# Optimization experiments

Hardware: AMD Instinct MI355X
Metric: run time of the kernel (lower is better)

## Reference

```python
import jax, jax.numpy as jnp
import numpy as np

B, N_PER, D = 128, 512, 128        # graphs, nodes per graph, feature width
N = B * N_PER                      # 65536 total nodes
E = 524288                         # total edges (avg degree 8)
KS = (410, 328, 263)               # ceil(0.8*512), ceil(0.8*410), ceil(0.8*328)


def setup_inputs() -> dict:
    key = jax.random.key(0)
    ks = jax.random.split(key, 20)
    p = lambda k, shape: jax.random.normal(k, shape, jnp.float32) * 0.05
    rng = np.random.default_rng(0)
    g = rng.integers(0, B, size=E)
    s = rng.integers(0, N_PER, size=E)
    t = rng.integers(0, N_PER, size=E)
    edge_index = jnp.asarray(np.stack([g * N_PER + s, g * N_PER + t]).astype(np.int32))
    inp = {
        'x': jax.random.normal(ks[0], (N, 1, D), jnp.float32),
        'edge_index': edge_index,
    }
    i = 1
    for l in (1, 2, 3):
        inp[f'conv{l}_wl'] = p(ks[i], (D, D)); i += 1   # SAGEConv lin_l (neighbors) weight
        inp[f'conv{l}_bl'] = p(ks[i], (D,));  i += 1   # SAGEConv lin_l bias
        inp[f'conv{l}_wr'] = p(ks[i], (D, D)); i += 1   # SAGEConv lin_r (root) weight
        inp[f'pool{l}_w'] = p(ks[i], (D,));   i += 1   # TopKPooling score vector
    inp['lin1_w'] = p(ks[13], (128, 256)); inp['lin1_b'] = p(ks[14], (128,))
    inp['lin2_w'] = p(ks[15], (64, 128));  inp['lin2_b'] = p(ks[16], (64,))
    inp['lin3_w'] = p(ks[17], (1, 64));    inp['lin3_b'] = p(ks[18], (1,))
    return inp


def _sage(x, node_mask, src, dst, wl, bl, wr):
    # SAGEConv, mean aggregation: lin_l(mean_{j->i} x_j) + lin_r(x_i)
    em = (node_mask[src] & node_mask[dst]).astype(x.dtype)   # [E] valid-edge mask
    msum = jax.ops.segment_sum(x[src] * em[:, None], dst, num_segments=N)
    deg = jax.ops.segment_sum(em, dst, num_segments=N)
    mean = msum / jnp.maximum(deg, 1.0)[:, None]
    return mean @ wl.T + bl + x @ wr.T


def _topk_pool(x, node_mask, w, k):
    # TopKPooling: score = x.w/||w||; keep top-k per graph; gate kept x by tanh(score)
    score = (x @ w) / (jnp.linalg.norm(w) + 1e-16)           # [N]
    score = jnp.where(node_mask, score, -jnp.inf)
    _, idx = jax.lax.top_k(score.reshape(B, N_PER), k)       # [B, k] within-graph ids
    nm = jnp.zeros((B, N_PER), bool).at[jnp.arange(B)[:, None], idx].set(True).reshape(-1)
    x = jnp.where(nm[:, None], x * jnp.tanh(score)[:, None], 0.0)
    return x, nm


def _readout(x, node_mask, k):
    # cat([global_max_pool, global_mean_pool]) over the k surviving nodes per graph
    xb = x.reshape(B, N_PER, -1)
    mb = node_mask.reshape(B, N_PER, 1)
    gmax = jnp.max(jnp.where(mb, xb, -jnp.inf), axis=1)
    gmean = jnp.sum(jnp.where(mb, xb, 0.0), axis=1) / k
    return jnp.concatenate([gmax, gmean], axis=1)            # [B, 2D]


def _forward(edge_index, x, conv1_wl, conv1_bl, conv1_wr, pool1_w,
             conv2_wl, conv2_bl, conv2_wr, pool2_w,
             conv3_wl, conv3_bl, conv3_wr, pool3_w,
             lin1_w, lin1_b, lin2_w, lin2_b, lin3_w, lin3_b):
    src, dst = edge_index[0], edge_index[1]
    h = x[:, 0, :]                                           # x.squeeze(1) -> [N, D]
    nm = jnp.ones((N,), bool)
    layers = ((conv1_wl, conv1_bl, conv1_wr, pool1_w),
              (conv2_wl, conv2_bl, conv2_wr, pool2_w),
              (conv3_wl, conv3_bl, conv3_wr, pool3_w))
    reads = []
    for (wl, bl, wr, pw), k in zip(layers, KS):
        h = jax.nn.relu(_sage(h, nm, src, dst, wl, bl, wr))
        h, nm = _topk_pool(h, nm, pw, k)
        reads.append(_readout(h, nm, float(k)))
    z = reads[0] + reads[1] + reads[2]                       # [B, 256]
    z = jax.nn.relu(z @ lin1_w.T + lin1_b)
    z = jax.nn.relu(z @ lin2_w.T + lin2_b)
    # dropout p=0.5 is a no-op at eval time
    return jax.nn.sigmoid(z @ lin3_w.T + lin3_b)[:, 0]       # [B]


def reference(x, edge_index, conv1_wl, conv1_bl, conv1_wr, pool1_w,
              conv2_wl, conv2_bl, conv2_wr, pool2_w,
              conv3_wl, conv3_bl, conv3_wr, pool3_w,
              lin1_w, lin1_b, lin2_w, lin2_b, lin3_w, lin3_b):
    return _forward(edge_index, x, conv1_wl, conv1_bl, conv1_wr, pool1_w,
                    conv2_wl, conv2_bl, conv2_wr, pool2_w,
                    conv3_wl, conv3_bl, conv3_wr, pool3_w,
                    lin1_w, lin1_b, lin2_w, lin2_b, lin3_w, lin3_b)
```

## Files before the change

kernel.cpp:

```cpp
#include <hip/hip_runtime.h>
#include <math.h>

#define NND 65536
#define NPER 512
#define NGR 128
#define DD 128
#define NED 524288

typedef __attribute__((ext_vector_type(8))) short short8;
typedef __attribute__((ext_vector_type(4))) float f32x4;

__device__ __forceinline__ unsigned short f2b(float f) {
  unsigned u = __float_as_uint(f);
  return (unsigned short)((u + 0x7FFFu + ((u >> 16) & 1u)) >> 16);
}
__device__ __forceinline__ float b2f(unsigned short h) {
  return __uint_as_float(((unsigned)h) << 16);
}


__global__ __launch_bounds__(256) void init_prepw_kernel(
    int* __restrict__ counts, float2* __restrict__ tm,
    const float* __restrict__ wl0, const float* __restrict__ wr0,
    const float* __restrict__ wl1, const float* __restrict__ wr1,
    const float* __restrict__ wl2, const float* __restrict__ wr2,
    unsigned short* __restrict__ Whi, unsigned short* __restrict__ Wlo) {
  const int bid = blockIdx.x;
  if (bid < 256) {
    int i = bid * 256 + threadIdx.x;
    counts[i] = 0;
    tm[i] = make_float2(1.f, 1.f);
    return;
  }
  const float* wls[3] = {wl0, wl1, wl2};
  const float* wrs[3] = {wr0, wr1, wr2};
  int e = (bid - 256) * 256 + threadIdx.x;
  int l = e >> 15;
  int o = e & 32767;
  int j = o & 7;
  int lane = (o >> 3) & 63;
  int nt = (o >> 9) & 7;
  int kc = o >> 12;
  int li = lane & 15, q = lane >> 4;
  int n = nt * 16 + li;
  int k = kc * 32 + q * 8 + j;
  const float* src = (k < 128) ? wls[l] : wrs[l];
  float v = src[n * DD + (k & 127)];
  unsigned short hi = f2b(v);
  float lo = v - b2f(hi);
  Whi[e] = hi;
  Wlo[e] = f2b(lo);
}

__global__ __launch_bounds__(256) void hist_kernel(const int* __restrict__ ei,
                                                   int* __restrict__ counts) {
  int e = blockIdx.x * 256 + threadIdx.x;
  atomicAdd(&counts[ei[NED + e]], 1);
}


__global__ __launch_bounds__(256) void scan1_kernel(const int* __restrict__ counts,
                                                    int* __restrict__ csum) {
  __shared__ int ws[4];
  const int b = blockIdx.x;
  const int t = threadIdx.x;
  const int4 v = ((const int4*)(counts + b * 1024))[t];
  int s = v.x + v.y + v.z + v.w;
#pragma unroll
  for (int o = 32; o > 0; o >>= 1) s += __shfl_down(s, o);
  if ((t & 63) == 0) ws[t >> 6] = s;
  __syncthreads();
  if (t == 0) csum[b] = ws[0] + ws[1] + ws[2] + ws[3];
}

__global__ __launch_bounds__(256) void scan2_kernel(const int* __restrict__ counts,
                                                    const int* __restrict__ csum,
                                                    int* __restrict__ off,
                                                    int* __restrict__ cursor) {
  __shared__ int s_part[256];
  __shared__ int s_base;
  const int b = blockIdx.x;
  const int t = threadIdx.x;
  const int4 v = ((const int4*)(counts + b * 1024))[t];
  const int s = v.x + v.y + v.z + v.w;
  s_part[t] = s;
  if (t < 64) {
    int val = (t < b) ? csum[t] : 0;
#pragma unroll
    for (int o = 32; o > 0; o >>= 1) val += __shfl_down(val, o);
    if (t == 0) s_base = val;
  }
  __syncthreads();
  for (int d = 1; d < 256; d <<= 1) {
    int val = (t >= d) ? s_part[t - d] : 0;
    __syncthreads();
    s_part[t] += val;
    __syncthreads();
  }
  const int excl = s_base + ((t == 0) ? 0 : s_part[t - 1]);
  int4 o4;
  o4.x = excl;
  o4.y = excl + v.x;
  o4.z = o4.y + v.y;
  o4.w = o4.z + v.z;
  ((int4*)(off + b * 1024))[t] = o4;
  ((int4*)(cursor + b * 1024))[t] = o4;
  if (b == 0 && t == 0) off[NND] = NED;
}

__global__ __launch_bounds__(256) void scatter_kernel(const int* __restrict__ ei,
                                                      int* __restrict__ cursor,
                                                      int* __restrict__ ssrc) {
  int e = blockIdx.x * 256 + threadIdx.x;
  int dst = ei[NED + e];
  int pos = atomicAdd(&cursor[dst], 1);
  ssrc[pos] = ei[e];
}


__global__ __launch_bounds__(256) void pe_kernel(const int* __restrict__ ssrc,
                                                 const float2* __restrict__ tm,
                                                 float* __restrict__ pet,
                                                 unsigned long long* __restrict__ plive) {
  const int e = blockIdx.x * 256 + threadIdx.x;
  const int s = ssrc[e];
  const float2 mt = tm[s];
  const int lv = (mt.x != 0.f) ? 1 : 0;
  pet[e] = lv ? mt.y : 0.f;
  const unsigned long long bl = __ballot(lv);
  if ((threadIdx.x & 63) == 0) plive[e >> 6] = bl;
}


template <int CM>
__global__ __launch_bounds__(256) void agg_kernel_t(
    const float* __restrict__ x, const float2* __restrict__ tm,
    const int* __restrict__ off, const int* __restrict__ ssrc,
    const float* __restrict__ pet, const unsigned long long* __restrict__ plive,
    unsigned short* __restrict__ mhi, unsigned short* __restrict__ mlo) {
  const int wave = threadIdx.x >> 6;
  const int lane = threadIdx.x & 63;
  const int half = lane >> 5;
  const int l = lane & 31;
  const int bid = blockIdx.x;
  const int xcd = bid & 7;
  const int slot = bid >> 3;
  const int graph = xcd * 16 + (slot >> 5);
  const int within = slot & 31;
  const int d0 = graph * NPER + within * 16 + wave * 4;

  int offv = 0;
  if (lane < 5) offv = off[d0 + lane];
  float deadv = 1.f;
  if (CM && lane < 4) deadv = tm[d0 + lane].x;
  const int b0 = __shfl(offv, 0);
  const int b1 = __shfl(offv, 1);
  const int b2 = __shfl(offv, 2);
  const int b3 = __shfl(offv, 3);
  const int e3 = __shfl(offv, 4);
  float dd[4];
  if (CM) {
    dd[0] = __shfl(deadv, 0);
    dd[1] = __shfl(deadv, 1);
    dd[2] = __shfl(deadv, 2);
    dd[3] = __shfl(deadv, 3);
  }
  const int begs[4] = {b0, b1, b2, b3};
  const int ends[4] = {b1, b2, b3, e3};

  float4 acc[4];
  int deg[4];
#pragma unroll
  for (int d = 0; d < 4; ++d) {
    acc[d] = make_float4(0.f, 0.f, 0.f, 0.f);
    deg[d] = 0;
  }

  for (int wbase = b0 & ~63; wbase < e3; wbase += 64) {
    const int sv = ssrc[wbase + lane];
    float tv = 0.f;
    unsigned long long lm = 0;
    if (CM) {
      tv = pet[wbase + lane];
      lm = plive[wbase >> 6];
    }

#pragma unroll
    for (int d = 0; d < 4; ++d) {
      if (CM && dd[d] == 0.f) continue;
      const int lo = max(begs[d], wbase);
      const int hi = min(ends[d], wbase + 64);
      if (lo >= hi) continue;
      const int j0 = lo - wbase;
      const int j1 = hi - wbase;
      if (CM) {
        const unsigned long long wm =
            (((j1 == 64) ? ~0ull : ((1ull << j1) - 1)) & ~((1ull << j0) - 1));
        deg[d] += (int)__popcll(lm & wm);
      } else {
        deg[d] += j1 - j0;
      }
      int j = j0 + half;
      for (; j + 6 < j1; j += 8) {
        const int s0 = __shfl(sv, j);
        const int s1 = __shfl(sv, j + 2);
        const int s2 = __shfl(sv, j + 4);
        const int s3 = __shfl(sv, j + 6);
        const float4 v0 = *(const float4*)(x + (size_t)s0 * DD + l * 4);
        const float4 v1 = *(const float4*)(x + (size_t)s1 * DD + l * 4);
        const float4 v2 = *(const float4*)(x + (size_t)s2 * DD + l * 4);
        const float4 v3 = *(const float4*)(x + (size_t)s3 * DD + l * 4);
        if (CM) {
          const float t0 = __shfl(tv, j), t1 = __shfl(tv, j + 2);
          const float t2 = __shfl(tv, j + 4), t3 = __shfl(tv, j + 6);
          acc[d].x += v0.x * t0 + v1.x * t1 + v2.x * t2 + v3.x * t3;
          acc[d].y += v0.y * t0 + v1.y * t1 + v2.y * t2 + v3.y * t3;
          acc[d].z += v0.z * t0 + v1.z * t1 + v2.z * t2 + v3.z * t3;
          acc[d].w += v0.w * t0 + v1.w * t1 + v2.w * t2 + v3.w * t3;
        } else {
          acc[d].x += v0.x + v1.x + v2.x + v3.x;
          acc[d].y += v0.y + v1.y + v2.y + v3.y;
          acc[d].z += v0.z + v1.z + v2.z + v3.z;
          acc[d].w += v0.w + v1.w + v2.w + v3.w;
        }
      }
      for (; j < j1; j += 2) {
        const int s = __shfl(sv, j);
        const float4 v = *(const float4*)(x + (size_t)s * DD + l * 4);
        if (CM) {
          const float t = __shfl(tv, j);
          acc[d].x += v.x * t;
          acc[d].y += v.y * t;
          acc[d].z += v.z * t;
          acc[d].w += v.w * t;
        } else {
          acc[d].x += v.x;
          acc[d].y += v.y;
          acc[d].z += v.z;
          acc[d].w += v.w;
        }
      }
    }
  }

#pragma unroll
  for (int d = 0; d < 4; ++d) {
    if (CM && dd[d] == 0.f) continue;
    float4 a = acc[d];
    a.x += __shfl(a.x, lane ^ 32);
    a.y += __shfl(a.y, lane ^ 32);
    a.z += __shfl(a.z, lane ^ 32);
    a.w += __shfl(a.w, lane ^ 32);
    if (lane < 32) {
      const float inv = 1.f / (float)max(deg[d], 1);
      float4 m;
      m.x = a.x * inv;
      m.y = a.y * inv;
      m.z = a.z * inv;
      m.w = a.w * inv;
      ushort4 hv, lv;
      hv.x = f2b(m.x); lv.x = f2b(m.x - b2f(hv.x));
      hv.y = f2b(m.y); lv.y = f2b(m.y - b2f(hv.y));
      hv.z = f2b(m.z); lv.z = f2b(m.z - b2f(hv.z));
      hv.w = f2b(m.w); lv.w = f2b(m.w - b2f(hv.w));
      const size_t ad = (size_t)(d0 + d) * DD + l * 4;
      *(ushort4*)(mhi + ad) = hv;
      *(ushort4*)(mlo + ad) = lv;
    }
  }
}


#define GBM 64

template <int SCALE>
__global__ __launch_bounds__(256) void gemm_kernel_t(
    const unsigned short* __restrict__ Amh, const unsigned short* __restrict__ Aml,
    const float* __restrict__ Ax, const float2* __restrict__ tmp,
    const unsigned short* __restrict__ Whi, const unsigned short* __restrict__ Wlo,
    const float* __restrict__ bias, const float* __restrict__ pw,
    float* __restrict__ outp, float* __restrict__ sraw) {
  __shared__ short Ah[4096];
  __shared__ short Al[4096];
  __shared__ float s_sp[4][GBM];
  const int tid = threadIdx.x;
  const int wv = tid >> 6;
  const int lane = tid & 63;
  const int q = lane >> 4;
  const int li = lane & 15;
  const int row0 = blockIdx.x * GBM;

  int sdst[2];
#pragma unroll
  for (int i = 0; i < 2; ++i) {
    const int id = tid + i * 256;
    const int r = id >> 3;
    const int kb = (id & 7) << 2;
    sdst[i] = ((r >> 4) * 64 + (kb >> 3) * 16 + (r & 15)) * 8 + (kb & 7);
  }

  f32x4 acc[4][2];
#pragma unroll
  for (int m = 0; m < 4; ++m)
#pragma unroll
    for (int n = 0; n < 2; ++n) acc[m][n] = (f32x4){0.f, 0.f, 0.f, 0.f};

  float4 pa[2];
  ushort4 pmh[2], pml[2];
  short8 pbh[2], pbl[2];

#define LOADA(KC)                                                                      \
  {                                                                                    \
    if ((KC) < 4) {                                                                    \
      const int cb = (KC)*32;                                                          \
      _Pragma("unroll") for (int i = 0; i < 2; ++i) {                                  \
        const int id = tid + i * 256;                                                  \
        const size_t ga = (size_t)(row0 + (id >> 3)) * DD + cb + ((id & 7) << 2);      \
        pmh[i] = *(const ushort4*)(Amh + ga);                                          \
        pml[i] = *(const ushort4*)(Aml + ga);                                          \
      }                                                                                \
    } else {                                                                           \
      const int cb = ((KC)&3) * 32;                                                    \
      _Pragma("unroll") for (int i = 0; i < 2; ++i) {                                  \
        const int id = tid + i * 256;                                                  \
        pa[i] = *(const float4*)(Ax + (size_t)(row0 + (id >> 3)) * DD + cb + ((id & 7) << 2)); \
        if (SCALE) {                                                                   \
          const float tt = tmp[row0 + (id >> 3)].y;                                    \
          pa[i].x *= tt; pa[i].y *= tt; pa[i].z *= tt; pa[i].w *= tt;                  \
        }                                                                              \
      }                                                                                \
    }                                                                                  \
  }
#define LOADB(KC)                                                                      \
  {                                                                                    \
    _Pragma("unroll") for (int n = 0; n < 2; ++n) {                                    \
      const int ga = (((KC)*8 + wv * 2 + n) * 64 + lane) * 8;                          \
      pbh[n] = *(const short8*)(Whi + ga);                                             \
      pbl[n] = *(const short8*)(Wlo + ga);                                             \
    }                                                                                  \
  }
#define STAGE(KC)                                                                      \
  {                                                                                    \
    short* Adh = Ah + ((KC)&1) * 2048;                                                 \
    short* Adl = Al + ((KC)&1) * 2048;                                                 \
    if ((KC) < 4) {                                                                    \
      _Pragma("unroll") for (int i = 0; i < 2; ++i) {                                  \
        *(ushort4*)(Adh + sdst[i]) = pmh[i];                                           \
        *(ushort4*)(Adl + sdst[i]) = pml[i];                                           \
      }                                                                                \
    } else {                                                                           \
      _Pragma("unroll") for (int i = 0; i < 2; ++i) {                                  \
        ushort4 hv, lv;                                                                \
        hv.x = f2b(pa[i].x); lv.x = f2b(pa[i].x - b2f(hv.x));                          \
        hv.y = f2b(pa[i].y); lv.y = f2b(pa[i].y - b2f(hv.y));                          \
        hv.z = f2b(pa[i].z); lv.z = f2b(pa[i].z - b2f(hv.z));                          \
        hv.w = f2b(pa[i].w); lv.w = f2b(pa[i].w - b2f(hv.w));                          \
        *(ushort4*)(Adh + sdst[i]) = hv;                                               \
        *(ushort4*)(Adl + sdst[i]) = lv;                                               \
      }                                                                                \
    }                                                                                  \
  }

  LOADA(0) LOADB(0)
  STAGE(0)
  LOADA(1)

#pragma unroll
  for (int kc = 0; kc < 8; ++kc) {
    short8 bh[2], bl[2];
    bh[0] = pbh[0]; bh[1] = pbh[1];
    bl[0] = pbl[0]; bl[1] = pbl[1];
    __syncthreads();
    short8 ah[4], al[4];
    const short* Ash = Ah + (kc & 1) * 2048;
    const short* Asl = Al + (kc & 1) * 2048;
#pragma unroll
    for (int m = 0; m < 4; ++m) {
      ah[m] = *(const short8*)(Ash + (m * 64 + lane) * 8);
      al[m] = *(const short8*)(Asl + (m * 64 + lane) * 8);
    }
    switch (kc) {
      case 0: STAGE(1) LOADB(1) LOADA(2) break;
      case 1: STAGE(2) LOADB(2) LOADA(3) break;
      case 2: STAGE(3) LOADB(3) LOADA(4) break;
      case 3: STAGE(4) LOADB(4) LOADA(5) break;
      case 4: STAGE(5) LOADB(5) LOADA(6) break;
      case 5: STAGE(6) LOADB(6) LOADA(7) break;
      case 6: STAGE(7) LOADB(7) break;
      default: break;
    }
#pragma unroll
    for (int m = 0; m < 4; ++m)
#pragma unroll
      for (int n = 0; n < 2; ++n) {
        acc[m][n] = __builtin_amdgcn_mfma_f32_16x16x32_bf16(ah[m], bh[n], acc[m][n], 0, 0, 0);
        acc[m][n] = __builtin_amdgcn_mfma_f32_16x16x32_bf16(ah[m], bl[n], acc[m][n], 0, 0, 0);
        acc[m][n] = __builtin_amdgcn_mfma_f32_16x16x32_bf16(al[m], bh[n], acc[m][n], 0, 0, 0);
      }
  }
#undef LOADA
#undef LOADB
#undef STAGE

  const int c0 = wv * 32 + li;
  const int c1 = wv * 32 + 16 + li;
  const float b0 = bias[c0], b1 = bias[c1];
  const float p0 = pw[c0], p1 = pw[c1];
  float sp[16];
#pragma unroll
  for (int m = 0; m < 4; ++m) {
#pragma unroll
    for (int i = 0; i < 4; ++i) {
      const int r = row0 + m * 16 + q * 4 + i;
      const float v0 = fmaxf(acc[m][0][i] + b0, 0.f);
      const float v1 = fmaxf(acc[m][1][i] + b1, 0.f);
      outp[(size_t)r * DD + c0] = v0;
      outp[(size_t)r * DD + c1] = v1;
      sp[m * 4 + i] = v0 * p0 + v1 * p1;
    }
  }
#pragma unroll
  for (int e = 0; e < 16; ++e) {
    sp[e] += __shfl_xor(sp[e], 1);
    sp[e] += __shfl_xor(sp[e], 2);
    sp[e] += __shfl_xor(sp[e], 4);
    sp[e] += __shfl_xor(sp[e], 8);
  }
  if (li == 0) {
#pragma unroll
    for (int e = 0; e < 16; ++e) s_sp[wv][(e >> 2) * 16 + q * 4 + (e & 3)] = sp[e];
  }
  __syncthreads();
  if (tid < GBM)
    sraw[row0 + tid] = s_sp[0][tid] + s_sp[1][tid] + s_sp[2][tid] + s_sp[3][tid];
}


__global__ __launch_bounds__(256) void pool_kernel(const float* __restrict__ h,
                                                   const float* __restrict__ sraw,
                                                   const float* __restrict__ pw,
                                                   const float2* __restrict__ tmP,
                                                   float2* __restrict__ tmN,
                                                   float* __restrict__ zp,
                                                   const int kk) {
  __shared__ float s_sc[NPER];
  __shared__ float s_t[128];
  __shared__ unsigned char s_sel[128];
  __shared__ int s_rk[256];
  __shared__ float4 red4[512];
  __shared__ float s_norm;
  const int b = blockIdx.x;
  const int g = b >> 2;
  const int q = b & 3;
  const int tid = threadIdx.x;
  const int lane = tid & 63;

  if (tid < 64) {
    const float v0 = pw[lane], v1 = pw[lane + 64];
    float p = v0 * v0 + v1 * v1;
#pragma unroll
    for (int o = 32; o > 0; o >>= 1) p += __shfl_down(p, o);
    if (lane == 0) s_norm = 1.f / (sqrtf(p) + 1e-16f);
  }
  __syncthreads();
  const float inv_norm = s_norm;
#pragma unroll
  for (int i = 0; i < 2; ++i) {
    const int n = tid + i * 256;
    const int node = g * NPER + n;
    s_sc[n] = (tmP[node].x != 0.f) ? sraw[node] * inv_norm : -INFINITY;
  }
  __syncthreads();

  {
    const int n = q * 128 + (tid & 127);
    const int jb = (tid >> 7) * 256;
    const float s = s_sc[n];
    int rank = 0;
    for (int j = jb; j < jb + 256; ++j) {
      const float sj = s_sc[j];
      rank += (sj > s || (sj == s && j < n)) ? 1 : 0;
    }
    s_rk[tid] = rank;
  }
  __syncthreads();
  if (tid < 128) {
    const int n = q * 128 + tid;
    const int rank = s_rk[tid] + s_rk[tid + 128];
    const int sel = (rank < kk) ? 1 : 0;
    const float s = s_sc[n];
    const float t = sel ? tanhf(s) : 0.f;
    tmN[g * NPER + n] = make_float2(sel ? 1.f : 0.f, t);
    s_sel[tid] = (unsigned char)sel;
    s_t[tid] = t;
  }
  __syncthreads();

  const int c = tid & 31;
  const int r = tid >> 5;
  float4 pmax = make_float4(-INFINITY, -INFINITY, -INFINITY, -INFINITY);
  float4 psum = make_float4(0.f, 0.f, 0.f, 0.f);
  const size_t nbase = (size_t)g * NPER + q * 128;
  const float4* h4 = (const float4*)h;
  for (int i = 0; i < 16; ++i) {
    const int nl = r + 8 * i;
    if (s_sel[nl]) {
      float4 v = h4[(nbase + nl) * 32 + c];
      const float t = s_t[nl];
      v.x *= t; v.y *= t; v.z *= t; v.w *= t;
      pmax.x = fmaxf(pmax.x, v.x);
      pmax.y = fmaxf(pmax.y, v.y);
      pmax.z = fmaxf(pmax.z, v.z);
      pmax.w = fmaxf(pmax.w, v.w);
      psum.x += v.x; psum.y += v.y; psum.z += v.z; psum.w += v.w;
    }
  }
  red4[r * 32 + c] = pmax;
  red4[256 + r * 32 + c] = psum;
  __syncthreads();
  if (tid < 32) {
    float4 m = red4[tid];
    float4 sm = red4[256 + tid];
#pragma unroll
    for (int rr = 1; rr < 8; ++rr) {
      const float4 a = red4[rr * 32 + tid];
      const float4 s2 = red4[256 + rr * 32 + tid];
      m.x = fmaxf(m.x, a.x); m.y = fmaxf(m.y, a.y);
      m.z = fmaxf(m.z, a.z); m.w = fmaxf(m.w, a.w);
      sm.x += s2.x; sm.y += s2.y; sm.z += s2.z; sm.w += s2.w;
    }
    *(float4*)(zp + (size_t)b * 256 + tid * 4) = m;
    *(float4*)(zp + (size_t)b * 256 + 128 + tid * 4) = sm;
  }
}


__global__ __launch_bounds__(128) void mlp_kernel(const float* __restrict__ zpart,
                                                  const float* __restrict__ w1,
                                                  const float* __restrict__ b1,
                                                  const float* __restrict__ w2,
                                                  const float* __restrict__ b2,
                                                  const float* __restrict__ w3,
                                                  const float* __restrict__ b3,
                                                  float* __restrict__ out,
                                                  const float ik0, const float ik1,
                                                  const float ik2) {
  __shared__ float z[256];
  __shared__ float h1[128];
  __shared__ float h2[64];
  const int g = blockIdx.x;
  const int t = threadIdx.x;
  const float iks[3] = {ik0, ik1, ik2};
  float zmax = 0.f, zmean = 0.f;
#pragma unroll
  for (int l = 0; l < 3; ++l) {
    const float* zp = zpart + ((size_t)l * 512 + g * 4) * 256;
    zmax += fmaxf(fmaxf(zp[t], zp[256 + t]), fmaxf(zp[512 + t], zp[768 + t]));
    zmean += (zp[128 + t] + zp[384 + t] + zp[640 + t] + zp[896 + t]) * iks[l];
  }
  z[t] = zmax;
  z[128 + t] = zmean;
  __syncthreads();
  float a = b1[t];
  for (int k = 0; k < 256; ++k) a = fmaf(z[k], w1[t * 256 + k], a);
  h1[t] = fmaxf(a, 0.f);
  __syncthreads();
  if (t < 64) {
    float a2 = b2[t];
    for (int k = 0; k < 128; ++k) a2 = fmaf(h1[k], w2[t * 128 + k], a2);
    h2[t] = fmaxf(a2, 0.f);
  }
  __syncthreads();
  if (t == 0) {
    float a3 = b3[0];
    for (int k = 0; k < 64; ++k) a3 = fmaf(h2[k], w3[k], a3);
    out[g] = 1.f / (1.f + expf(-a3));
  }
}


extern "C" void kernel_launch(void* const* d_in, const int* in_sizes, int n_in,
                              void* d_out, int out_size, void* d_ws, size_t ws_size,
                              hipStream_t stream) {
  (void)in_sizes; (void)n_in; (void)out_size; (void)ws_size;
  const float* x_in = (const float*)d_in[0];
  const int* ei = (const int*)d_in[1];
  const float* wl[3] = {(const float*)d_in[2], (const float*)d_in[6], (const float*)d_in[10]};
  const float* cbl[3] = {(const float*)d_in[3], (const float*)d_in[7], (const float*)d_in[11]};
  const float* wr[3] = {(const float*)d_in[4], (const float*)d_in[8], (const float*)d_in[12]};
  const float* pw[3] = {(const float*)d_in[5], (const float*)d_in[9], (const float*)d_in[13]};
  const float* l1w = (const float*)d_in[14];
  const float* l1b = (const float*)d_in[15];
  const float* l2w = (const float*)d_in[16];
  const float* l2b = (const float*)d_in[17];
  const float* l3w = (const float*)d_in[18];
  const float* l3b = (const float*)d_in[19];
  float* out = (float*)d_out;

  char* w = (char*)d_ws;
  int* counts = (int*)(w + 0 * (1 << 20));
  int* off = (int*)(w + 1 * (1 << 20));
  int* csum = (int*)(w + 1 * (1 << 20) + (1 << 19));
  int* cursor = (int*)(w + 2 * (1 << 20));
  float* sraw = (float*)(w + 2 * (1 << 20));
  float2* tmA = (float2*)(w + 3 * (1 << 20));
  float2* tmB = (float2*)(w + 3 * (1 << 20) + (1 << 19));
  float* zpart = (float*)(w + 4 * (1 << 20));
  unsigned short* Whi = (unsigned short*)(w + 5 * (1 << 20) + (1 << 19));
  unsigned short* Wlo = (unsigned short*)(w + 5 * (1 << 20) + 3 * (1 << 18));
  int* ssrc = (int*)(w + 6 * (1 << 20));
  unsigned short* mhi = (unsigned short*)(w + (size_t)8 * (1 << 20));
  unsigned short* mlo = (unsigned short*)(w + (size_t)24 * (1 << 20));
  float* hA = (float*)(w + (size_t)40 * (1 << 20));
  float* hB = (float*)(w + (size_t)72 * (1 << 20));
  float* pet = (float*)(w + (size_t)104 * (1 << 20));
  unsigned long long* plive = (unsigned long long*)(w + (size_t)107 * (1 << 20));

  init_prepw_kernel<<<640, 256, 0, stream>>>(counts, tmA, wl[0], wr[0], wl[1], wr[1],
                                             wl[2], wr[2], Whi, Wlo);
  hist_kernel<<<NED / 256, 256, 0, stream>>>(ei, counts);
  scan1_kernel<<<64, 256, 0, stream>>>(counts, csum);
  scan2_kernel<<<64, 256, 0, stream>>>(counts, csum, off, cursor);
  scatter_kernel<<<NED / 256, 256, 0, stream>>>(ei, cursor, ssrc);

  const int ks[3] = {410, 328, 263};
  const float* xl = x_in;
  float* houts[3] = {hA, hB, hA};
  float2* tprev[3] = {tmA, tmB, tmA};
  float2* tnext[3] = {tmB, tmA, tmB};
  for (int l = 0; l < 3; ++l) {
    float* hout = houts[l];
    if (l == 0) {
      agg_kernel_t<0><<<4096, 256, 0, stream>>>(xl, tprev[l], off, ssrc, pet, plive,
                                                mhi, mlo);
      gemm_kernel_t<0><<<NND / GBM, 256, 0, stream>>>(mhi, mlo, xl, tprev[l],
                                                      Whi + (size_t)l * 32768,
                                                      Wlo + (size_t)l * 32768, cbl[l], pw[l],
                                                      hout, sraw);
    } else {
      pe_kernel<<<NED / 256, 256, 0, stream>>>(ssrc, tprev[l], pet, plive);
      agg_kernel_t<1><<<4096, 256, 0, stream>>>(xl, tprev[l], off, ssrc, pet, plive,
                                                mhi, mlo);
      gemm_kernel_t<1><<<NND / GBM, 256, 0, stream>>>(mhi, mlo, xl, tprev[l],
                                                      Whi + (size_t)l * 32768,
                                                      Wlo + (size_t)l * 32768, cbl[l], pw[l],
                                                      hout, sraw);
    }
    pool_kernel<<<NGR * 4, 256, 0, stream>>>(hout, sraw, pw[l], tprev[l], tnext[l],
                                             zpart + (size_t)l * 512 * 256, ks[l]);
    xl = hout;
  }
  mlp_kernel<<<NGR, 128, 0, stream>>>(zpart, l1w, l1b, l2w, l2b, l3w, l3b, out,
                                      1.f / 410.f, 1.f / 328.f, 1.f / 263.f);
}
```

Measured before the change: 366.7 us.

## Fuse neighbor mean aggregation into SAGE GEMM kernel via shared memory

Merges the aggregation kernel and the GEMM kernel into one kernel. Each block gathers neighbor means for 64 rows and writes the bf16 hi/lo split straight into LDS in MFMA fragment layout, so the global round trip through the mhi/mlo buffers and one launch per layer go away. Each wave now handles 16 destination nodes with 16 float4 accumulators, which raises register pressure, and the grid shrinks from 4096 to 1024 blocks with more LDS per block, which may lower occupancy and gather latency hiding. The per-node dead-node skip is also dropped, so dead destinations are still aggregated.

```diff
diff --git a/kernel.cpp b/kernel.cpp
--- a/kernel.cpp
+++ b/kernel.cpp
@@ -133,50 +133,52 @@
 
 
 template <int CM>
-__global__ __launch_bounds__(256) void agg_kernel_t(
-    const float* __restrict__ x, const float2* __restrict__ tm,
+__global__ __launch_bounds__(256) void fused_kernel_t(
+    const float* __restrict__ x, const float2* __restrict__ tmp,
     const int* __restrict__ off, const int* __restrict__ ssrc,
     const float* __restrict__ pet, const unsigned long long* __restrict__ plive,
-    unsigned short* __restrict__ mhi, unsigned short* __restrict__ mlo) {
-  const int wave = threadIdx.x >> 6;
-  const int lane = threadIdx.x & 63;
+    const unsigned short* __restrict__ Whi, const unsigned short* __restrict__ Wlo,
+    const float* __restrict__ bias, const float* __restrict__ pw,
+    float* __restrict__ outp, float* __restrict__ sraw) {
+  __shared__ short Mh[8192];
+  __shared__ short Ml[8192];
+  __shared__ short Ah[4096];
+  __shared__ short Al[4096];
+  __shared__ float s_sp[4][64];
+  const int tid = threadIdx.x;
+  const int wv = tid >> 6;
+  const int lane = tid & 63;
   const int half = lane >> 5;
   const int l = lane & 31;
+  const int q = lane >> 4;
+  const int li = lane & 15;
   const int bid = blockIdx.x;
   const int xcd = bid & 7;
-  const int slot = bid >> 3;
-  const int graph = xcd * 16 + (slot >> 5);
-  const int within = slot & 31;
-  const int d0 = graph * NPER + within * 16 + wave * 4;
-
+  const int idx = bid >> 3;
+  const int graph = xcd * 16 + (idx >> 3);
+  const int row0 = graph * NPER + (idx & 7) * 64;
+
+  const int d0 = row0 + wv * 16;
   int offv = 0;
-  if (lane < 5) offv = off[d0 + lane];
-  float deadv = 1.f;
-  if (CM && lane < 4) deadv = tm[d0 + lane].x;
-  const int b0 = __shfl(offv, 0);
-  const int b1 = __shfl(offv, 1);
-  const int b2 = __shfl(offv, 2);
-  const int b3 = __shfl(offv, 3);
-  const int e3 = __shfl(offv, 4);
-  float dd[4];
-  if (CM) {
-    dd[0] = __shfl(deadv, 0);
-    dd[1] = __shfl(deadv, 1);
-    dd[2] = __shfl(deadv, 2);
-    dd[3] = __shfl(deadv, 3);
-  }
-  const int begs[4] = {b0, b1, b2, b3};
-  const int ends[4] = {b1, b2, b3, e3};
-
-  float4 acc[4];
-  int deg[4];
-#pragma unroll
-  for (int d = 0; d < 4; ++d) {
-    acc[d] = make_float4(0.f, 0.f, 0.f, 0.f);
+  if (lane < 17) offv = off[d0 + lane];
+  int begs[16], ends[16];
+#pragma unroll
+  for (int d = 0; d < 16; ++d) {
+    begs[d] = __builtin_amdgcn_readfirstlane(__shfl(offv, d));
+    ends[d] = __builtin_amdgcn_readfirstlane(__shfl(offv, d + 1));
+  }
+  const int b0 = begs[0];
+  const int eN = ends[15];
+
+  float4 macc[16];
+  int deg[16];
+#pragma unroll
+  for (int d = 0; d < 16; ++d) {
+    macc[d] = make_float4(0.f, 0.f, 0.f, 0.f);
     deg[d] = 0;
   }
 
-  for (int wbase = b0 & ~63; wbase < e3; wbase += 64) {
+  for (int wbase = b0 & ~63; wbase < eN; wbase += 64) {
     const int sv = ssrc[wbase + lane];
     float tv = 0.f;
     unsigned long long lm = 0;
@@ -184,10 +186,8 @@
       tv = pet[wbase + lane];
       lm = plive[wbase >> 6];
     }
-
-#pragma unroll
-    for (int d = 0; d < 4; ++d) {
-      if (CM && dd[d] == 0.f) continue;
+#pragma unroll
+    for (int d = 0; d < 16; ++d) {
       const int lo = max(begs[d], wbase);
       const int hi = min(ends[d], wbase + 64);
       if (lo >= hi) continue;
@@ -213,15 +213,15 @@
         if (CM) {
           const float t0 = __shfl(tv, j), t1 = __shfl(tv, j + 2);
           const float t2 = __shfl(tv, j + 4), t3 = __shfl(tv, j + 6);
-          acc[d].x += v0.x * t0 + v1.x * t1 + v2.x * t2 + v3.x * t3;
-          acc[d].y += v0.y * t0 + v1.y * t1 + v2.y * t2 + v3.y * t3;
-          acc[d].z += v0.z * t0 + v1.z * t1 + v2.z * t2 + v3.z * t3;
-          acc[d].w += v0.w * t0 + v1.w * t1 + v2.w * t2 + v3.w * t3;
+          macc[d].x += v0.x * t0 + v1.x * t1 + v2.x * t2 + v3.x * t3;
+          macc[d].y += v0.y * t0 + v1.y * t1 + v2.y * t2 + v3.y * t3;
+          macc[d].z += v0.z * t0 + v1.z * t1 + v2.z * t2 + v3.z * t3;
+          macc[d].w += v0.w * t0 + v1.w * t1 + v2.w * t2 + v3.w * t3;
         } else {
-          acc[d].x += v0.x + v1.x + v2.x + v3.x;
-          acc[d].y += v0.y + v1.y + v2.y + v3.y;
-          acc[d].z += v0.z + v1.z + v2.z + v3.z;
-          acc[d].w += v0.w + v1.w + v2.w + v3.w;
+          macc[d].x += v0.x + v1.x + v2.x + v3.x;
+          macc[d].y += v0.y + v1.y + v2.y + v3.y;
+          macc[d].z += v0.z + v1.z + v2.z + v3.z;
+          macc[d].w += v0.w + v1.w + v2.w + v3.w;
         }
       }
       for (; j < j1; j += 2) {
@@ -229,24 +229,23 @@
         const float4 v = *(const float4*)(x + (size_t)s * DD + l * 4);
         if (CM) {
           const float t = __shfl(tv, j);
-          acc[d].x += v.x * t;
-          acc[d].y += v.y * t;
-          acc[d].z += v.z * t;
-          acc[d].w += v.w * t;
+          macc[d].x += v.x * t;
+          macc[d].y += v.y * t;
+          macc[d].z += v.z * t;
+          macc[d].w += v.w * t;
         } else {
-          acc[d].x += v.x;
-          acc[d].y += v.y;
-          acc[d].z += v.z;
-          acc[d].w += v.w;
+          macc[d].x += v.x;
+          macc[d].y += v.y;
+          macc[d].z += v.z;
+          macc[d].w += v.w;
         }
       }
     }
   }
 
 #pragma unroll
-  for (int d = 0; d < 4; ++d) {
-    if (CM && dd[d] == 0.f) continue;
-    float4 a = acc[d];
+  for (int d = 0; d < 16; ++d) {
+    float4 a = macc[d];
     a.x += __shfl(a.x, lane ^ 32);
     a.y += __shfl(a.y, lane ^ 32);
     a.z += __shfl(a.z, lane ^ 32);
@@ -263,32 +262,11 @@
       hv.y = f2b(m.y); lv.y = f2b(m.y - b2f(hv.y));
       hv.z = f2b(m.z); lv.z = f2b(m.z - b2f(hv.z));
       hv.w = f2b(m.w); lv.w = f2b(m.w - b2f(hv.w));
-      const size_t ad = (size_t)(d0 + d) * DD + l * 4;
-      *(ushort4*)(mhi + ad) = hv;
-      *(ushort4*)(mlo + ad) = lv;
-    }
-  }
-}
-
-
-#define GBM 64
-
-template <int SCALE>
-__global__ __launch_bounds__(256) void gemm_kernel_t(
-    const unsigned short* __restrict__ Amh, const unsigned short* __restrict__ Aml,
-    const float* __restrict__ Ax, const float2* __restrict__ tmp,
-    const unsigned short* __restrict__ Whi, const unsigned short* __restrict__ Wlo,
-    const float* __restrict__ bias, const float* __restrict__ pw,
-    float* __restrict__ outp, float* __restrict__ sraw) {
-  __shared__ short Ah[4096];
-  __shared__ short Al[4096];
-  __shared__ float s_sp[4][GBM];
-  const int tid = threadIdx.x;
-  const int wv = tid >> 6;
-  const int lane = tid & 63;
-  const int q = lane >> 4;
-  const int li = lane & 15;
-  const int row0 = blockIdx.x * GBM;
+      const int ad = (wv * 256 + (l >> 1) * 16 + d) * 8 + (l & 1) * 4;
+      *(ushort4*)(Mh + ad) = hv;
+      *(ushort4*)(Ml + ad) = lv;
+    }
+  }
 
   int sdst[2];
 #pragma unroll
@@ -299,38 +277,7 @@
     sdst[i] = ((r >> 4) * 64 + (kb >> 3) * 16 + (r & 15)) * 8 + (kb & 7);
   }
 
-  f32x4 acc[4][2];
-#pragma unroll
-  for (int m = 0; m < 4; ++m)
-#pragma unroll
-    for (int n = 0; n < 2; ++n) acc[m][n] = (f32x4){0.f, 0.f, 0.f, 0.f};
-
-  float4 pa[2];
-  ushort4 pmh[2], pml[2];
   short8 pbh[2], pbl[2];
-
-#define LOADA(KC)                                                                      \
-  {                                                                                    \
-    if ((KC) < 4) {                                                                    \
-      const int cb = (KC)*32;                                                          \
-      _Pragma("unroll") for (int i = 0; i < 2; ++i) {                                  \
-        const int id = tid + i * 256;                                                  \
-        const size_t ga = (size_t)(row0 + (id >> 3)) * DD + cb + ((id & 7) << 2);      \
-        pmh[i] = *(const ushort4*)(Amh + ga);                                          \
-        pml[i] = *(const ushort4*)(Aml + ga);                                          \
-      }                                                                                \
-    } else {                                                                           \
-      const int cb = ((KC)&3) * 32;                                                    \
-      _Pragma("unroll") for (int i = 0; i < 2; ++i) {                                  \
-        const int id = tid + i * 256;                                                  \
-        pa[i] = *(const float4*)(Ax + (size_t)(row0 + (id >> 3)) * DD + cb + ((id & 7) << 2)); \
-        if (SCALE) {                                                                   \
-          const float tt = tmp[row0 + (id >> 3)].y;                                    \
-          pa[i].x *= tt; pa[i].y *= tt; pa[i].z *= tt; pa[i].w *= tt;                  \
-        }                                                                              \
-      }                                                                                \
-    }                                                                                  \
-  }
 #define LOADB(KC)                                                                      \
   {                                                                                    \
     _Pragma("unroll") for (int n = 0; n < 2; ++n) {                                    \
@@ -339,72 +286,104 @@
       pbl[n] = *(const short8*)(Wlo + ga);                                             \
     }                                                                                  \
   }
-#define STAGE(KC)                                                                      \
+#define LOADAX(KC, PA)                                                                 \
+  {                                                                                    \
+    const int cb = ((KC)&3) * 32;                                                      \
+    _Pragma("unroll") for (int i = 0; i < 2; ++i) {                                    \
+      const int id = tid + i * 256;                                                    \
+      PA[i] = *(const float4*)(x + (size_t)(row0 + (id >> 3)) * DD + cb + ((id & 7) << 2)); \
+      if (CM) {                                                                        \
+        const float tt = tmp[row0 + (id >> 3)].y;                                      \
+        PA[i].x *= tt; PA[i].y *= tt; PA[i].z *= tt; PA[i].w *= tt;                    \
+      }                                                                                \
+    }                                                                                  \
+  }
+#define STAGEX(KC, PA)                                                                 \
   {                                                                                    \
     short* Adh = Ah + ((KC)&1) * 2048;                                                 \
     short* Adl = Al + ((KC)&1) * 2048;                                                 \
-    if ((KC) < 4) {                                                                    \
-      _Pragma("unroll") for (int i = 0; i < 2; ++i) {                                  \
-        *(ushort4*)(Adh + sdst[i]) = pmh[i];                                           \
-        *(ushort4*)(Adl + sdst[i]) = pml[i];                                           \
-      }                                                                                \
-    } else {                                                                           \
-      _Pragma("unroll") for (int i = 0; i < 2; ++i) {                                  \
-        ushort4 hv, lv;                                                                \
-        hv.x = f2b(pa[i].x); lv.x = f2b(pa[i].x - b2f(hv.x));                          \
-        hv.y = f2b(pa[i].y); lv.y = f2b(pa[i].y - b2f(hv.y));                          \
-        hv.z = f2b(pa[i].z); lv.z = f2b(pa[i].z - b2f(hv.z));                          \
-        hv.w = f2b(pa[i].w); lv.w = f2b(pa[i].w - b2f(hv.w));                          \
-        *(ushort4*)(Adh + sdst[i]) = hv;                                               \
-        *(ushort4*)(Adl + sdst[i]) = lv;                                               \
-      }                                                                                \
+    _Pragma("unroll") for (int i = 0; i < 2; ++i) {                                    \
+      ushort4 hv, lv;                                                                  \
+      hv.x = f2b(PA[i].x); lv.x = f2b(PA[i].x - b2f(hv.x));                            \
+      hv.y = f2b(PA[i].y); lv.y = f2b(PA[i].y - b2f(hv.y));                            \
+      hv.z = f2b(PA[i].z); lv.z = f2b(PA[i].z - b2f(hv.z));                            \
+      hv.w = f2b(PA[i].w); lv.w = f2b(PA[i].w - b2f(hv.w));                            \
+      *(ushort4*)(Adh + sdst[i]) = hv;                                                 \
+      *(ushort4*)(Adl + sdst[i]) = lv;                                                 \
     }                                                                                  \
   }
-
-  LOADA(0) LOADB(0)
-  STAGE(0)
-  LOADA(1)
-
-#pragma unroll
-  for (int kc = 0; kc < 8; ++kc) {
-    short8 bh[2], bl[2];
-    bh[0] = pbh[0]; bh[1] = pbh[1];
-    bl[0] = pbl[0]; bl[1] = pbl[1];
-    __syncthreads();
-    short8 ah[4], al[4];
-    const short* Ash = Ah + (kc & 1) * 2048;
-    const short* Asl = Al + (kc & 1) * 2048;
-#pragma unroll
-    for (int m = 0; m < 4; ++m) {
-      ah[m] = *(const short8*)(Ash + (m * 64 + lane) * 8);
-      al[m] = *(const short8*)(Asl + (m * 64 + lane) * 8);
-    }
-    switch (kc) {
-      case 0: STAGE(1) LOADB(1) LOADA(2) break;
-      case 1: STAGE(2) LOADB(2) LOADA(3) break;
-      case 2: STAGE(3) LOADB(3) LOADA(4) break;
-      case 3: STAGE(4) LOADB(4) LOADA(5) break;
-      case 4: STAGE(5) LOADB(5) LOADA(6) break;
-      case 5: STAGE(6) LOADB(6) LOADA(7) break;
-      case 6: STAGE(7) LOADB(7) break;
-      default: break;
-    }
-#pragma unroll
-    for (int m = 0; m < 4; ++m)
-#pragma unroll
-      for (int n = 0; n < 2; ++n) {
-        acc[m][n] = __builtin_amdgcn_mfma_f32_16x16x32_bf16(ah[m], bh[n], acc[m][n], 0, 0, 0);
-        acc[m][n] = __builtin_amdgcn_mfma_f32_16x16x32_bf16(ah[m], bl[n], acc[m][n], 0, 0, 0);
-        acc[m][n] = __builtin_amdgcn_mfma_f32_16x16x32_bf16(al[m], bh[n], acc[m][n], 0, 0, 0);
-      }
-  }
-#undef LOADA
+#define MFMA_KC(AH, AL)                                                                \
+  _Pragma("unroll") for (int m = 0; m < 4; ++m)                                        \
+      _Pragma("unroll") for (int n = 0; n < 2; ++n) {                                  \
+    acc[m][n] = __builtin_amdgcn_mfma_f32_16x16x32_bf16(AH[m], bh[n], acc[m][n], 0, 0, 0); \
+    acc[m][n] = __builtin_amdgcn_mfma_f32_16x16x32_bf16(AH[m], bl[n], acc[m][n], 0, 0, 0); \
+    acc[m][n] = __builtin_amdgcn_mfma_f32_16x16x32_bf16(AL[m], bh[n], acc[m][n], 0, 0, 0); \
+  }
+#define GRAB_B()                                                                       \
+  short8 bh[2], bl[2];                                                                 \
+  bh[0] = pbh[0]; bh[1] = pbh[1];                                                      \
+  bl[0] = pbl[0]; bl[1] = pbl[1];
+#define READ_MEAN(KC, AH, AL)                                                          \
+  short8 AH[4], AL[4];                                                                 \
+  _Pragma("unroll") for (int m = 0; m < 4; ++m) {                                      \
+    const int ra = (m * 256 + ((KC)*4 + q) * 16 + li) * 8;                             \
+    AH[m] = *(const short8*)(Mh + ra);                                                 \
+    AL[m] = *(const short8*)(Ml + ra);                                                 \
+  }
+#define READ_STAGE(KC, AH, AL)                                                         \
+  short8 AH[4], AL[4];                                                                 \
+  {                                                                                    \
+    const short* Ash = Ah + ((KC)&1) * 2048;                                           \
+    const short* Asl = Al + ((KC)&1) * 2048;                                           \
+    _Pragma("unroll") for (int m = 0; m < 4; ++m) {                                    \
+      AH[m] = *(const short8*)(Ash + (m * 64 + lane) * 8);                             \
+      AL[m] = *(const short8*)(Asl + (m * 64 + lane) * 8);                             \
+    }                                                                                  \
+  }
+
+  f32x4 acc[4][2];
+#pragma unroll
+  for (int m = 0; m < 4; ++m)
+#pragma unroll
+    for (int n = 0; n < 2; ++n) acc[m][n] = (f32x4){0.f, 0.f, 0.f, 0.f};
+
+  float4 pa4[2], pa5[2], pa6[2], pa7[2];
+  LOADB(0)
+  LOADAX(4, pa4)
+  LOADAX(5, pa5)
+  __syncthreads();
+
+  STAGEX(4, pa4)
+  STAGEX(5, pa5)
+  LOADAX(6, pa6)
+  LOADAX(7, pa7)
+
+  {
+    { GRAB_B() LOADB(1) READ_MEAN(0, ah, al) MFMA_KC(ah, al) }
+    { GRAB_B() LOADB(2) READ_MEAN(1, ah, al) MFMA_KC(ah, al) }
+    { GRAB_B() LOADB(3) READ_MEAN(2, ah, al) MFMA_KC(ah, al) }
+    { GRAB_B() LOADB(4) READ_MEAN(3, ah, al) MFMA_KC(ah, al) }
+  }
+  __syncthreads();
+  { GRAB_B() LOADB(5) READ_STAGE(4, ah, al) MFMA_KC(ah, al) }
+  __syncthreads();
+  { GRAB_B() LOADB(6) READ_STAGE(5, ah, al) STAGEX(6, pa6) MFMA_KC(ah, al) }
+  __syncthreads();
+  { GRAB_B() LOADB(7) READ_STAGE(6, ah, al) STAGEX(7, pa7) MFMA_KC(ah, al) }
+  __syncthreads();
+  { GRAB_B() READ_STAGE(7, ah, al) MFMA_KC(ah, al) }
+
 #undef LOADB
-#undef STAGE
+#undef LOADAX
+#undef STAGEX
+#undef MFMA_KC
+#undef GRAB_B
+#undef READ_MEAN
+#undef READ_STAGE
 
   const int c0 = wv * 32 + li;
   const int c1 = wv * 32 + 16 + li;
-  const float b0 = bias[c0], b1 = bias[c1];
+  const float bs0 = bias[c0], bs1 = bias[c1];
   const float p0 = pw[c0], p1 = pw[c1];
   float sp[16];
 #pragma unroll
@@ -412,8 +391,8 @@
 #pragma unroll
     for (int i = 0; i < 4; ++i) {
       const int r = row0 + m * 16 + q * 4 + i;
-      const float v0 = fmaxf(acc[m][0][i] + b0, 0.f);
-      const float v1 = fmaxf(acc[m][1][i] + b1, 0.f);
+      const float v0 = fmaxf(acc[m][0][i] + bs0, 0.f);
+      const float v1 = fmaxf(acc[m][1][i] + bs1, 0.f);
       outp[(size_t)r * DD + c0] = v0;
       outp[(size_t)r * DD + c1] = v1;
       sp[m * 4 + i] = v0 * p0 + v1 * p1;
@@ -431,7 +410,7 @@
     for (int e = 0; e < 16; ++e) s_sp[wv][(e >> 2) * 16 + q * 4 + (e & 3)] = sp[e];
   }
   __syncthreads();
-  if (tid < GBM)
+  if (tid < 64)
     sraw[row0 + tid] = s_sp[0][tid] + s_sp[1][tid] + s_sp[2][tid] + s_sp[3][tid];
 }
 
@@ -609,8 +588,6 @@
   unsigned short* Whi = (unsigned short*)(w + 5 * (1 << 20) + (1 << 19));
   unsigned short* Wlo = (unsigned short*)(w + 5 * (1 << 20) + 3 * (1 << 18));
   int* ssrc = (int*)(w + 6 * (1 << 20));
-  unsigned short* mhi = (unsigned short*)(w + (size_t)8 * (1 << 20));
-  unsigned short* mlo = (unsigned short*)(w + (size_t)24 * (1 << 20));
   float* hA = (float*)(w + (size_t)40 * (1 << 20));
   float* hB = (float*)(w + (size_t)72 * (1 << 20));
   float* pet = (float*)(w + (size_t)104 * (1 << 20));
@@ -631,20 +608,16 @@
   for (int l = 0; l < 3; ++l) {
     float* hout = houts[l];
     if (l == 0) {
-      agg_kernel_t<0><<<4096, 256, 0, stream>>>(xl, tprev[l], off, ssrc, pet, plive,
-                                                mhi, mlo);
-      gemm_kernel_t<0><<<NND / GBM, 256, 0, stream>>>(mhi, mlo, xl, tprev[l],
-                                                      Whi + (size_t)l * 32768,
-                                                      Wlo + (size_t)l * 32768, cbl[l], pw[l],
-                                                      hout, sraw);
+      fused_kernel_t<0><<<1024, 256, 0, stream>>>(xl, tprev[l], off, ssrc, pet, plive,
+                                                  Whi + (size_t)l * 32768,
+                                                  Wlo + (size_t)l * 32768, cbl[l], pw[l],
+                                                  hout, sraw);
     } else {
       pe_kernel<<<NED / 256, 256, 0, stream>>>(ssrc, tprev[l], pet, plive);
-      agg_kernel_t<1><<<4096, 256, 0, stream>>>(xl, tprev[l], off, ssrc, pet, plive,
-                                                mhi, mlo);
-      gemm_kernel_t<1><<<NND / GBM, 256, 0, stream>>>(mhi, mlo, xl, tprev[l],
-                                                      Whi + (size_t)l * 32768,
-                                                      Wlo + (size_t)l * 32768, cbl[l], pw[l],
-                                                      hout, sraw);
+      fused_kernel_t<1><<<1024, 256, 0, stream>>>(xl, tprev[l], off, ssrc, pet, plive,
+                                                  Whi + (size_t)l * 32768,
+                                                  Wlo + (size_t)l * 32768, cbl[l], pw[l],
+                                                  hout, sraw);
     }
     pool_kernel<<<NGR * 4, 256, 0, stream>>>(hout, sraw, pw[l], tprev[l], tnext[l],
                                              zpart + (size_t)l * 512 * 256, ks[l]);
```

Result: slower. 403.3 us (+10.0%).
